# Kernel optimization log

Hardware: AMD Instinct MI355X
Metric: run time of the kernel (lower is better)

Reference implementation:

```python
import jax, jax.numpy as jnp
import numpy as np

B, S, D, H = 4, 2048, 512, 8
DEPTH = D // H


def setup_inputs() -> dict:
    key = jax.random.key(0)
    ks = jax.random.split(key, 12)
    s = 0.02
    return {
        "q": jax.random.normal(ks[0], (B, S, D), jnp.float32),
        "k": jax.random.normal(ks[1], (B, S, D), jnp.float32),
        "v": jax.random.normal(ks[2], (B, S, D), jnp.float32),
        "mask": jax.random.randint(ks[3], (B, 1, 1, S), 0, 2, jnp.int32),
        "wq": jax.random.normal(ks[4], (D, D), jnp.float32) * s,
        "bq": jnp.zeros((D,), jnp.float32),
        "wk": jax.random.normal(ks[5], (D, D), jnp.float32) * s,
        "bk": jnp.zeros((D,), jnp.float32),
        "wv": jax.random.normal(ks[6], (D, D), jnp.float32) * s,
        "bv": jnp.zeros((D,), jnp.float32),
        "wo": jax.random.normal(ks[7], (D, D), jnp.float32) * s,
        "bo": jnp.zeros((D,), jnp.float32),
    }


def _split_heads(x):
    # [B,S,D] -> [B,H,S,depth]
    b = x.shape[0]
    return x.reshape(b, -1, H, DEPTH).transpose(0, 2, 1, 3)


def reference(q, k, v, mask, wq, bq, wk, bk, wv, bv, wo, bo):
    qh = _split_heads(q @ wq + bq)
    kh = _split_heads(k @ wk + bk)
    vh = _split_heads(v @ wv + bv)
    scale = 1.0 / jnp.sqrt(jnp.float32(DEPTH))
    logits = jnp.einsum("bhqd,bhkd->bhqk", qh, kh) * scale
    logits = logits + mask.astype(jnp.float32) * -1e9
    attn = jax.nn.softmax(logits, axis=-1)  # [B,H,Sq,Sk]
    out = jnp.einsum("bhqk,bhkd->bhqd", attn, vh)
    out = out.transpose(0, 2, 1, 3).reshape(q.shape[0], -1, D)
    out = out @ wo + bo
    return out, attn
```

## Files before the change

kernel.cpp:

```cpp
#include <hip/hip_runtime.h>

#define B_ 4
#define S_ 2048
#define D_ 512
#define H_ 8
#define DP_ 64
#define NT_ (S_/64)

typedef __attribute__((ext_vector_type(4))) float f32x4;
typedef __attribute__((ext_vector_type(8))) short short8;
typedef __attribute__((ext_vector_type(4))) int i32x4;

__device__ __forceinline__ short f2bf(float f){
  unsigned u = __float_as_uint(f);
  u += 0x7fff + ((u >> 16) & 1);
  return (short)(u >> 16);
}

__device__ __forceinline__ int cvtpk(float lo, float hi){
  int r;
  asm("v_cvt_pk_bf16_f32 %0, %1, %2" : "=v"(r) : "v"(lo), "v"(hi));
  return r;
}

#define SWZ(r, kb) ((r)*64 + ((kb) ^ (((r)&7)<<3)))
#define F2(r) ((((r)&3)) | ((((r)>>3)&1)<<2))
#define SWZ2(r, kb) ((r)*64 + ((kb) ^ (F2(r)<<3)))

#define WAITV(N) do{ asm volatile("s_waitcnt vmcnt(" #N ")" ::: "memory"); }while(0)
#define BAR() do{ __builtin_amdgcn_s_barrier(); __builtin_amdgcn_sched_barrier(0); }while(0)

template<int NC>
__device__ __forceinline__ void stage_swz(const short* __restrict__ g, int rowStride,
                                          short* shbase, int w, int l){
  #pragma unroll
  for(int i = 0; i < NC; ++i){
    int byte = (w*NC + i)*1024 + l*16;
    int row = byte >> 7;
    int gs = ((byte >> 4) & 7) ^ (row & 7);
    const short* src = g + (size_t)row*rowStride + gs*8;
    __builtin_amdgcn_global_load_lds((const __attribute__((address_space(1))) void*)src,
        (__attribute__((address_space(3))) void*)(shbase + (w*NC + i)*512), 16, 0, 0);
  }
}
template<int NC>
__device__ __forceinline__ void stage_swz2(const short* __restrict__ g, int rowStride,
                                           short* shbase, int w, int l){
  #pragma unroll
  for(int i = 0; i < NC; ++i){
    int byte = (w*NC + i)*1024 + l*16;
    int row = byte >> 7;
    int gs = ((byte >> 4) & 7) ^ F2(row);
    const short* src = g + (size_t)row*rowStride + gs*8;
    __builtin_amdgcn_global_load_lds((const __attribute__((address_space(1))) void*)src,
        (__attribute__((address_space(3))) void*)(shbase + (w*NC + i)*512), 16, 0, 0);
  }
}

__global__ __launch_bounds__(256) void k_pre(const int* __restrict__ mask,
        const float* __restrict__ w0, const float* __restrict__ w1,
        const float* __restrict__ w2, const float* __restrict__ w3,
        short* __restrict__ wT, float* __restrict__ mb){
  __shared__ float tt[32][33];
  const int bi = blockIdx.x, t = threadIdx.x;
  if(bi < 1024){
    const int z = bi >> 8;
    const float* w = z == 0 ? w0 : z == 1 ? w1 : z == 2 ? w2 : w3;
    short* wt = wT + z * 262144;
    const int bxy = bi & 255;
    const int bx = (bxy & 15) * 32, by = (bxy >> 4) * 32;
    const int tx = t & 31, ty = t >> 5;
    #pragma unroll
    for(int i = 0; i < 32; i += 8) tt[ty + i][tx] = w[(by + ty + i) * D_ + bx + tx];
    __syncthreads();
    #pragma unroll
    for(int i = 0; i < 32; i += 8) wt[(bx + ty + i) * D_ + by + tx] = f2bf(tt[tx][ty + i]);
  } else {
    int i = (bi - 1024) * 256 + t;
    mb[i] = mask[i] ? -1.0e9f : 0.0f;
  }
}

__global__ __launch_bounds__(256) void k_gemm_qkv(const float* __restrict__ qf,
        const float* __restrict__ kf, const float* __restrict__ vf,
        const short* __restrict__ WTall, const float* __restrict__ b0,
        const float* __restrict__ b1, const float* __restrict__ b2,
        short* __restrict__ qh, short* __restrict__ kh, short* __restrict__ vvt){
  __shared__ __align__(16) short As[8192];
  __shared__ __align__(16) short Bs[8192];
  const int z = blockIdx.z;
  const float* X = z == 0 ? qf : (z == 1 ? kf : vf);
  const short* WT = WTall + (size_t)z * (D_*D_);
  const float* bias = z==0 ? b0 : (z==1 ? b1 : b2);
  const int t = threadIdx.x, l = t & 63, w = t >> 6;
  const int lr = l & 15, lg = l >> 4;
  const int m0 = blockIdx.x * 128, n0 = blockIdx.y * 128;
  const int wr = w >> 1, wc = w & 1;
  const float* Xb = X + (size_t)m0 * D_;
  const short* Wb = WT + (size_t)n0 * D_;
  f32x4 acc[4][4] = {};
  for(int kt = 0; kt < D_ / 64; ++kt){
    #pragma unroll
    for(int i = 0; i < 4; ++i){
      int e = t + 256 * i;
      int row = e >> 3, c8 = (e & 7) * 8;
      const float* src = Xb + (size_t)row * D_ + kt * 64 + c8;
      float4 f0 = *reinterpret_cast<const float4*>(src);
      float4 f1 = *reinterpret_cast<const float4*>(src + 4);
      i32x4 pk;
      pk[0] = cvtpk(f0.x, f0.y); pk[1] = cvtpk(f0.z, f0.w);
      pk[2] = cvtpk(f1.x, f1.y); pk[3] = cvtpk(f1.z, f1.w);
      *reinterpret_cast<i32x4*>(&As[SWZ(row, c8)]) = pk;
    }
    stage_swz<4>(Wb + kt*64, D_, Bs, w, l);
    __syncthreads();
    #pragma unroll
    for(int ks = 0; ks < 2; ++ks){
      const int kb = ks*32 + lg*8;
      short8 a[4], b[4];
      #pragma unroll
      for(int mt = 0; mt < 4; ++mt)
        a[mt] = *reinterpret_cast<const short8*>(&As[SWZ(wr*64 + mt*16 + lr, kb)]);
      #pragma unroll
      for(int nt = 0; nt < 4; ++nt)
        b[nt] = *reinterpret_cast<const short8*>(&Bs[SWZ(wc*64 + nt*16 + lr, kb)]);
      __builtin_amdgcn_s_setprio(1);
      #pragma unroll
      for(int mt = 0; mt < 4; ++mt)
        #pragma unroll
        for(int nt = 0; nt < 4; ++nt)
          acc[mt][nt] = __builtin_amdgcn_mfma_f32_16x16x32_bf16(a[mt], b[nt], acc[mt][nt], 0, 0, 0);
      __builtin_amdgcn_s_setprio(0);
    }
    __syncthreads();
  }
  #pragma unroll
  for(int mt = 0; mt < 4; ++mt){
    #pragma unroll
    for(int nt = 0; nt < 4; ++nt){
      const int n = n0 + wc*64 + nt*16 + lr;
      const int m4 = m0 + wr*64 + mt*16 + lg*4;
      float vals[4];
      #pragma unroll
      for(int r = 0; r < 4; ++r) vals[r] = acc[mt][nt][r] + bias[n];
      if(z == 2){
        short4 pv4;
        pv4.x = f2bf(vals[0]); pv4.y = f2bf(vals[1]); pv4.z = f2bf(vals[2]); pv4.w = f2bf(vals[3]);
        *reinterpret_cast<short4*>(&vvt[
            (((size_t)((m4 >> 11) * H_ + (n >> 6))) * DP_ + (n & 63)) * S_ + (m4 & 2047)]) = pv4;
      } else {
        short* dst = z == 0 ? qh : kh;
        #pragma unroll
        for(int r = 0; r < 4; ++r){
          int m = m4 + r;
          dst[(((size_t)((m >> 11) * H_ + (n >> 6))) * S_ + (m & 2047)) * DP_ + (n & 63)] = f2bf(vals[r]);
        }
      }
    }
  }
}

__global__ __launch_bounds__(256) void k_gemm_out(const short* __restrict__ X,
        const short* __restrict__ WT, const float* __restrict__ bias,
        float* __restrict__ Out){
  __shared__ __align__(16) short As[8192];
  __shared__ __align__(16) short Bs[8192];
  const int t = threadIdx.x, l = t & 63, w = t >> 6;
  const int lr = l & 15, lg = l >> 4;
  const int m0 = blockIdx.x * 128, n0 = blockIdx.y * 128;
  const int wr = w >> 1, wc = w & 1;
  const short* Xb = X + (size_t)m0 * D_;
  const short* Wb = WT + (size_t)n0 * D_;
  f32x4 acc[4][4] = {};
  for(int kt = 0; kt < D_ / 64; ++kt){
    stage_swz<4>(Xb + kt*64, D_, As, w, l);
    stage_swz<4>(Wb + kt*64, D_, Bs, w, l);
    __syncthreads();
    #pragma unroll
    for(int ks = 0; ks < 2; ++ks){
      const int kb = ks*32 + lg*8;
      short8 a[4], b[4];
      #pragma unroll
      for(int mt = 0; mt < 4; ++mt)
        a[mt] = *reinterpret_cast<const short8*>(&As[SWZ(wr*64 + mt*16 + lr, kb)]);
      #pragma unroll
      for(int nt = 0; nt < 4; ++nt)
        b[nt] = *reinterpret_cast<const short8*>(&Bs[SWZ(wc*64 + nt*16 + lr, kb)]);
      __builtin_amdgcn_s_setprio(1);
      #pragma unroll
      for(int mt = 0; mt < 4; ++mt)
        #pragma unroll
        for(int nt = 0; nt < 4; ++nt)
          acc[mt][nt] = __builtin_amdgcn_mfma_f32_16x16x32_bf16(a[mt], b[nt], acc[mt][nt], 0, 0, 0);
      __builtin_amdgcn_s_setprio(0);
    }
    __syncthreads();
  }
  #pragma unroll
  for(int mt = 0; mt < 4; ++mt){
    #pragma unroll
    for(int nt = 0; nt < 4; ++nt){
      const int n = n0 + wc*64 + nt*16 + lr;
      const int m4 = m0 + wr*64 + mt*16 + lg*4;
      #pragma unroll
      for(int r = 0; r < 4; ++r)
        Out[(size_t)(m4 + r) * D_ + n] = acc[mt][nt][r] + bias[n];
    }
  }
}

__global__ __launch_bounds__(512, 4) void k_attn(const short* __restrict__ qh,
                                                 const short* __restrict__ kh,
                                                 const short* __restrict__ vt,
                                                 const float* __restrict__ mb,
                                                 float* __restrict__ attn,
                                                 short* __restrict__ ctx){
  __shared__ __align__(16) short Sh[36864];
  const int t = threadIdx.x, l = t & 63, w = t >> 6;
  const int lr = l & 15, lg = l >> 4;
  int lin = blockIdx.y * 16 + blockIdx.x;
  int sw = (lin & 7) * 64 + (lin >> 3);
  const int bh = sw >> 4, b = bh >> 3, h = bh & 7;
  const int q0 = (sw & 15) * 128;
  const short* Qb = qh + (size_t)bh * S_ * DP_ + (size_t)q0 * DP_;
  const short* Kb = kh + (size_t)bh * S_ * DP_;
  const short* Vtb = vt + (size_t)bh * DP_ * S_;
  const float* Mbb = mb + b * S_;
  float* Mlds = (float*)Sh;
  short* KA = Sh + 4096;
  short* KB = Sh + 4096;
  short* VB = Sh + 20480;
  short* Qs = Sh + 28672;
  const float scale = 0.125f;

  __builtin_amdgcn_global_load_lds(
      (const __attribute__((address_space(1))) void*)(Mbb + w*256 + l*4),
      (__attribute__((address_space(3))) void*)(Mlds + w*256 + l*4), 16, 0, 0);
  stage_swz2<2>(Qb, DP_, Qs, w, l);
  stage_swz2<1>(Kb,            DP_, KA,            w, l);
  stage_swz2<1>(Kb + 4096,     DP_, KA + 4096,     w, l);
  stage_swz2<1>(Kb + 2*4096,   DP_, KA + 2*4096,   w, l);
  stage_swz2<1>(Kb + 3*4096,   DP_, KA + 3*4096,   w, l);
  WAITV(4); BAR();
  short8 bq0, bq1;
  {
    int r = w * 16 + lr;
    bq0 = *reinterpret_cast<const short8*>(&Qs[SWZ2(r, lg * 8)]);
    bq1 = *reinterpret_cast<const short8*>(&Qs[SWZ2(r, 32 + lg * 8)]);
  }
  const int grow = ((lr >> 2) << 3) + (lr & 3);

  float ps = 0.f;
  for(int i = 0; i < NT_/2; ++i){
    if(i < NT_/2 - 1){ WAITV(2); } else { WAITV(0); }
    BAR();
    if(i + 2 < NT_/2){
      int tfa = 2*i + 4, tfb = 2*i + 5;
      stage_swz2<1>(Kb + (size_t)tfa * 4096, DP_, KA + (tfa % 6) * 4096, w, l);
      stage_swz2<1>(Kb + (size_t)tfb * 4096, DP_, KA + (tfb % 6) * 4096, w, l);
    }
    #pragma unroll
    for(int tt = 0; tt < 2; ++tt){
      const int kt = 2*i + tt;
      const short* Kc = KA + (kt % 6) * 4096;
      const float* Ml = Mlds + kt * 64;
      #pragma unroll
      for(int st = 0; st < 4; ++st){
        const int ks = st >> 1, h4 = st & 1;
        const int row = grow + h4 * 4 + ks * 32;
        const int mcol = ks * 32 + h4 * 4 + lg * 8;
        const float4 mv = *(const float4*)&Ml[mcol];
        short8 ak0 = *reinterpret_cast<const short8*>(&Kc[SWZ2(row, lg * 8)]);
        short8 ak1 = *reinterpret_cast<const short8*>(&Kc[SWZ2(row, 32 + lg * 8)]);
        __builtin_amdgcn_s_setprio(1);
        f32x4 c = {};
        c = __builtin_amdgcn_mfma_f32_16x16x32_bf16(ak0, bq0, c, 0, 0, 0);
        c = __builtin_amdgcn_mfma_f32_16x16x32_bf16(ak1, bq1, c, 0, 0, 0);
        __builtin_amdgcn_s_setprio(0);
        ps += __expf(__builtin_fmaf(c[0], scale, mv.x));
        ps += __expf(__builtin_fmaf(c[1], scale, mv.y));
        ps += __expf(__builtin_fmaf(c[2], scale, mv.z));
        ps += __expf(__builtin_fmaf(c[3], scale, mv.w));
      }
    }
  }
  ps += __shfl_xor(ps, 16, 64);
  ps += __shfl_xor(ps, 32, 64);
  const float rinv = 1.f / ps;

  BAR();
  stage_swz2<1>(Kb,          DP_, KB,          w, l);
  stage_swz2<1>(Kb + 4096,   DP_, KB + 4096,   w, l);
  stage_swz2<1>(Vtb,         S_,  VB,          w, l);
  stage_swz2<1>(Vtb + 64,    S_,  VB + 4096,   w, l);
  stage_swz2<1>(Kb + 2*4096, DP_, KB + 2*4096, w, l);
  stage_swz2<1>(Kb + 3*4096, DP_, KB + 3*4096, w, l);
  stage_swz2<1>(Vtb + 2*64,  S_,  VB + 2*4096, w, l);
  stage_swz2<1>(Vtb + 3*64,  S_,  VB + 3*4096, w, l);

  f32x4 o[4] = {};
  for(int i = 0; i < NT_/2; ++i){
    if(i == 0){ WAITV(4); } else { WAITV(8); }
    BAR();
    if(i >= 1 && i + 1 < NT_/2){
      int tfa = 2*i + 2, tfb = 2*i + 3;
      stage_swz2<1>(Kb + (size_t)tfa * 4096, DP_, KB + (tfa & 3) * 4096, w, l);
      stage_swz2<1>(Kb + (size_t)tfb * 4096, DP_, KB + (tfb & 3) * 4096, w, l);
      stage_swz2<1>(Vtb + (size_t)tfa * 64,  S_,  VB + (tfa & 3) * 4096, w, l);
      stage_swz2<1>(Vtb + (size_t)tfb * 64,  S_,  VB + (tfb & 3) * 4096, w, l);
    }
    #pragma unroll
    for(int tt = 0; tt < 2; ++tt){
      const int kt = 2*i + tt;
      const short* Kc = KB + (kt & 3) * 4096;
      const short* Vc = VB + (kt & 3) * 4096;
      const float* Ml = Mlds + kt * 64;
      const int q = q0 + w * 16 + lr;
      i32x4 pav[2];
      #pragma unroll
      for(int st = 0; st < 4; ++st){
        const int ks = st >> 1, h4 = st & 1;
        const int row = grow + h4 * 4 + ks * 32;
        const int mcol = ks * 32 + h4 * 4 + lg * 8;
        const float4 mv = *(const float4*)&Ml[mcol];
        short8 ak0 = *reinterpret_cast<const short8*>(&Kc[SWZ2(row, lg * 8)]);
        short8 ak1 = *reinterpret_cast<const short8*>(&Kc[SWZ2(row, 32 + lg * 8)]);
        __builtin_amdgcn_s_setprio(1);
        f32x4 c = {};
        c = __builtin_amdgcn_mfma_f32_16x16x32_bf16(ak0, bq0, c, 0, 0, 0);
        c = __builtin_amdgcn_mfma_f32_16x16x32_bf16(ak1, bq1, c, 0, 0, 0);
        __builtin_amdgcn_s_setprio(0);
        float4 pw;
        pw.x = __expf(__builtin_fmaf(c[0], scale, mv.x)) * rinv;
        pw.y = __expf(__builtin_fmaf(c[1], scale, mv.y)) * rinv;
        pw.z = __expf(__builtin_fmaf(c[2], scale, mv.z)) * rinv;
        pw.w = __expf(__builtin_fmaf(c[3], scale, mv.w)) * rinv;
        *reinterpret_cast<float4*>(&attn[((size_t)bh * S_ + q) * S_ + kt * 64 + mcol]) = pw;
        pav[ks][h4 * 2 + 0] = cvtpk(pw.x, pw.y);
        pav[ks][h4 * 2 + 1] = cvtpk(pw.z, pw.w);
      }
      #pragma unroll
      for(int ks = 0; ks < 2; ++ks){
        short8 pa = __builtin_bit_cast(short8, pav[ks]);
        __builtin_amdgcn_s_setprio(1);
        #pragma unroll
        for(int dt = 0; dt < 4; ++dt){
          short8 vb = *reinterpret_cast<const short8*>(&Vc[SWZ2(dt * 16 + lr, ks * 32 + lg * 8)]);
          o[dt] = __builtin_amdgcn_mfma_f32_16x16x32_bf16(pa, vb, o[dt], 0, 0, 0);
        }
        __builtin_amdgcn_s_setprio(0);
      }
    }
  }
  #pragma unroll
  for(int dt = 0; dt < 4; ++dt){
    #pragma unroll
    for(int r = 0; r < 4; ++r){
      int q = q0 + w * 16 + lg * 4 + r;
      int dd = h * 64 + dt * 16 + lr;
      ctx[((size_t)b * S_ + q) * D_ + dd] = f2bf(o[dt][r]);
    }
  }
}

extern "C" void kernel_launch(void* const* d_in, const int* in_sizes, int n_in,
                              void* d_out, int out_size, void* d_ws, size_t ws_size,
                              hipStream_t stream){
  const float* q  = (const float*)d_in[0];
  const float* k  = (const float*)d_in[1];
  const float* v  = (const float*)d_in[2];
  const int* mask = (const int*)d_in[3];
  const float* wq = (const float*)d_in[4];
  const float* bq = (const float*)d_in[5];
  const float* wk = (const float*)d_in[6];
  const float* bk = (const float*)d_in[7];
  const float* wv = (const float*)d_in[8];
  const float* bv = (const float*)d_in[9];
  const float* wo = (const float*)d_in[10];
  const float* bo = (const float*)d_in[11];

  float* out  = (float*)d_out;
  float* attn = out + (size_t)B_ * S_ * D_;

  char* ws = (char*)d_ws;
  short* qh  = (short*)(ws);
  short* kh  = (short*)(ws + 8388608);
  short* vvt = (short*)(ws + 16777216);
  short* ctx = (short*)(ws + 25165824);
  short* wT  = (short*)(ws + 33554432);
  float* mb  = (float*)(ws + 33554432 + 4 * 524288);

  hipLaunchKernelGGL(k_pre, dim3(1056), dim3(256), 0, stream,
                     mask, wq, wk, wv, wo, wT, mb);

  hipLaunchKernelGGL(k_gemm_qkv, dim3(64, 4, 3), dim3(256), 0, stream,
                     q, k, v, wT, bq, bk, bv, qh, kh, vvt);

  hipLaunchKernelGGL(k_attn, dim3(16, 32), dim3(512), 0, stream, qh, kh, vvt, mb, attn, ctx);

  hipLaunchKernelGGL(k_gemm_out, dim3(64, 4), dim3(256), 0, stream, ctx, wT + 3 * 262144, bo, out);
}
```

Before: 223.9 us.

## Process two query sub-tiles per wave in attention to reuse K/V tiles

Each attention block now covers 256 queries instead of 128, with every wave computing two 16-row query sub-tiles that share the same K and V fragments read from LDS. This halves the number of blocks and the K/V global-to-LDS staging per query, cutting memory traffic for keys and values. In exchange, register use roughly doubles for accumulators, the launch bound drops to 2 blocks per CU, and only 256 blocks remain, which may hurt occupancy and latency hiding. The kernel is dominated by writing the large attn probability matrix, so the gain from reuse may be limited.

```diff
diff --git a/kernel.cpp b/kernel.cpp
--- a/kernel.cpp
+++ b/kernel.cpp
@@ -209,19 +209,19 @@
   }
 }
 
-__global__ __launch_bounds__(512, 4) void k_attn(const short* __restrict__ qh,
+__global__ __launch_bounds__(512, 2) void k_attn(const short* __restrict__ qh,
                                                  const short* __restrict__ kh,
                                                  const short* __restrict__ vt,
                                                  const float* __restrict__ mb,
                                                  float* __restrict__ attn,
                                                  short* __restrict__ ctx){
-  __shared__ __align__(16) short Sh[36864];
+  __shared__ __align__(16) short Sh[45056];
   const int t = threadIdx.x, l = t & 63, w = t >> 6;
   const int lr = l & 15, lg = l >> 4;
-  int lin = blockIdx.y * 16 + blockIdx.x;
-  int sw = (lin & 7) * 64 + (lin >> 3);
-  const int bh = sw >> 4, b = bh >> 3, h = bh & 7;
-  const int q0 = (sw & 15) * 128;
+  int lin = blockIdx.y * 8 + blockIdx.x;
+  int sw = (lin & 7) * 32 + (lin >> 3);
+  const int bh = sw >> 3, b = bh >> 3, h = bh & 7;
+  const int q0 = (sw & 7) * 256;
   const short* Qb = qh + (size_t)bh * S_ * DP_ + (size_t)q0 * DP_;
   const short* Kb = kh + (size_t)bh * S_ * DP_;
   const short* Vtb = vt + (size_t)bh * DP_ * S_;
@@ -236,21 +236,22 @@
   __builtin_amdgcn_global_load_lds(
       (const __attribute__((address_space(1))) void*)(Mbb + w*256 + l*4),
       (__attribute__((address_space(3))) void*)(Mlds + w*256 + l*4), 16, 0, 0);
-  stage_swz2<2>(Qb, DP_, Qs, w, l);
-  stage_swz2<1>(Kb,            DP_, KA,            w, l);
-  stage_swz2<1>(Kb + 4096,     DP_, KA + 4096,     w, l);
-  stage_swz2<1>(Kb + 2*4096,   DP_, KA + 2*4096,   w, l);
-  stage_swz2<1>(Kb + 3*4096,   DP_, KA + 3*4096,   w, l);
+  stage_swz2<4>(Qb, DP_, Qs, w, l);
+  stage_swz2<1>(Kb,          DP_, KA,          w, l);
+  stage_swz2<1>(Kb + 4096,   DP_, KA + 4096,   w, l);
+  stage_swz2<1>(Kb + 2*4096, DP_, KA + 2*4096, w, l);
+  stage_swz2<1>(Kb + 3*4096, DP_, KA + 3*4096, w, l);
   WAITV(4); BAR();
-  short8 bq0, bq1;
-  {
-    int r = w * 16 + lr;
-    bq0 = *reinterpret_cast<const short8*>(&Qs[SWZ2(r, lg * 8)]);
-    bq1 = *reinterpret_cast<const short8*>(&Qs[SWZ2(r, 32 + lg * 8)]);
+  short8 bq[2][2];
+  #pragma unroll
+  for(int qs = 0; qs < 2; ++qs){
+    int r = w * 32 + qs * 16 + lr;
+    bq[qs][0] = *reinterpret_cast<const short8*>(&Qs[SWZ2(r, lg * 8)]);
+    bq[qs][1] = *reinterpret_cast<const short8*>(&Qs[SWZ2(r, 32 + lg * 8)]);
   }
   const int grow = ((lr >> 2) << 3) + (lr & 3);
 
-  float ps = 0.f;
+  float ps[2] = {0.f, 0.f};
   for(int i = 0; i < NT_/2; ++i){
     if(i < NT_/2 - 1){ WAITV(2); } else { WAITV(0); }
     BAR();
@@ -273,20 +274,29 @@
         short8 ak0 = *reinterpret_cast<const short8*>(&Kc[SWZ2(row, lg * 8)]);
         short8 ak1 = *reinterpret_cast<const short8*>(&Kc[SWZ2(row, 32 + lg * 8)]);
         __builtin_amdgcn_s_setprio(1);
-        f32x4 c = {};
-        c = __builtin_amdgcn_mfma_f32_16x16x32_bf16(ak0, bq0, c, 0, 0, 0);
-        c = __builtin_amdgcn_mfma_f32_16x16x32_bf16(ak1, bq1, c, 0, 0, 0);
+        f32x4 c0 = {}, c1 = {};
+        c0 = __builtin_amdgcn_mfma_f32_16x16x32_bf16(ak0, bq[0][0], c0, 0, 0, 0);
+        c0 = __builtin_amdgcn_mfma_f32_16x16x32_bf16(ak1, bq[0][1], c0, 0, 0, 0);
+        c1 = __builtin_amdgcn_mfma_f32_16x16x32_bf16(ak0, bq[1][0], c1, 0, 0, 0);
+        c1 = __builtin_amdgcn_mfma_f32_16x16x32_bf16(ak1, bq[1][1], c1, 0, 0, 0);
         __builtin_amdgcn_s_setprio(0);
-        ps += __expf(__builtin_fmaf(c[0], scale, mv.x));
-        ps += __expf(__builtin_fmaf(c[1], scale, mv.y));
-        ps += __expf(__builtin_fmaf(c[2], scale, mv.z));
-        ps += __expf(__builtin_fmaf(c[3], scale, mv.w));
+        ps[0] += __expf(__builtin_fmaf(c0[0], scale, mv.x));
+        ps[0] += __expf(__builtin_fmaf(c0[1], scale, mv.y));
+        ps[0] += __expf(__builtin_fmaf(c0[2], scale, mv.z));
+        ps[0] += __expf(__builtin_fmaf(c0[3], scale, mv.w));
+        ps[1] += __expf(__builtin_fmaf(c1[0], scale, mv.x));
+        ps[1] += __expf(__builtin_fmaf(c1[1], scale, mv.y));
+        ps[1] += __expf(__builtin_fmaf(c1[2], scale, mv.z));
+        ps[1] += __expf(__builtin_fmaf(c1[3], scale, mv.w));
       }
     }
   }
-  ps += __shfl_xor(ps, 16, 64);
-  ps += __shfl_xor(ps, 32, 64);
-  const float rinv = 1.f / ps;
+  #pragma unroll
+  for(int qs = 0; qs < 2; ++qs){
+    ps[qs] += __shfl_xor(ps[qs], 16, 64);
+    ps[qs] += __shfl_xor(ps[qs], 32, 64);
+  }
+  const float rinv0 = 1.f / ps[0], rinv1 = 1.f / ps[1];
 
   BAR();
   stage_swz2<1>(Kb,          DP_, KB,          w, l);
@@ -298,9 +308,9 @@
   stage_swz2<1>(Vtb + 2*64,  S_,  VB + 2*4096, w, l);
   stage_swz2<1>(Vtb + 3*64,  S_,  VB + 3*4096, w, l);
 
-  f32x4 o[4] = {};
+  f32x4 o[2][4] = {};
   for(int i = 0; i < NT_/2; ++i){
-    if(i == 0){ WAITV(4); } else { WAITV(8); }
+    if(i == 0){ WAITV(4); } else { WAITV(16); }
     BAR();
     if(i >= 1 && i + 1 < NT_/2){
       int tfa = 2*i + 2, tfb = 2*i + 3;
@@ -315,8 +325,7 @@
       const short* Kc = KB + (kt & 3) * 4096;
       const short* Vc = VB + (kt & 3) * 4096;
       const float* Ml = Mlds + kt * 64;
-      const int q = q0 + w * 16 + lr;
-      i32x4 pav[2];
+      i32x4 pav[2][2];
       #pragma unroll
       for(int st = 0; st < 4; ++st){
         const int ks = st >> 1, h4 = st & 1;
@@ -326,39 +335,54 @@
         short8 ak0 = *reinterpret_cast<const short8*>(&Kc[SWZ2(row, lg * 8)]);
         short8 ak1 = *reinterpret_cast<const short8*>(&Kc[SWZ2(row, 32 + lg * 8)]);
         __builtin_amdgcn_s_setprio(1);
-        f32x4 c = {};
-        c = __builtin_amdgcn_mfma_f32_16x16x32_bf16(ak0, bq0, c, 0, 0, 0);
-        c = __builtin_amdgcn_mfma_f32_16x16x32_bf16(ak1, bq1, c, 0, 0, 0);
+        f32x4 c0 = {}, c1 = {};
+        c0 = __builtin_amdgcn_mfma_f32_16x16x32_bf16(ak0, bq[0][0], c0, 0, 0, 0);
+        c0 = __builtin_amdgcn_mfma_f32_16x16x32_bf16(ak1, bq[0][1], c0, 0, 0, 0);
+        c1 = __builtin_amdgcn_mfma_f32_16x16x32_bf16(ak0, bq[1][0], c1, 0, 0, 0);
+        c1 = __builtin_amdgcn_mfma_f32_16x16x32_bf16(ak1, bq[1][1], c1, 0, 0, 0);
         __builtin_amdgcn_s_setprio(0);
-        float4 pw;
-        pw.x = __expf(__builtin_fmaf(c[0], scale, mv.x)) * rinv;
-        pw.y = __expf(__builtin_fmaf(c[1], scale, mv.y)) * rinv;
-        pw.z = __expf(__builtin_fmaf(c[2], scale, mv.z)) * rinv;
-        pw.w = __expf(__builtin_fmaf(c[3], scale, mv.w)) * rinv;
-        *reinterpret_cast<float4*>(&attn[((size_t)bh * S_ + q) * S_ + kt * 64 + mcol]) = pw;
-        pav[ks][h4 * 2 + 0] = cvtpk(pw.x, pw.y);
-        pav[ks][h4 * 2 + 1] = cvtpk(pw.z, pw.w);
+        float4 pw0, pw1;
+        pw0.x = __expf(__builtin_fmaf(c0[0], scale, mv.x)) * rinv0;
+        pw0.y = __expf(__builtin_fmaf(c0[1], scale, mv.y)) * rinv0;
+        pw0.z = __expf(__builtin_fmaf(c0[2], scale, mv.z)) * rinv0;
+        pw0.w = __expf(__builtin_fmaf(c0[3], scale, mv.w)) * rinv0;
+        pw1.x = __expf(__builtin_fmaf(c1[0], scale, mv.x)) * rinv1;
+        pw1.y = __expf(__builtin_fmaf(c1[1], scale, mv.y)) * rinv1;
+        pw1.z = __expf(__builtin_fmaf(c1[2], scale, mv.z)) * rinv1;
+        pw1.w = __expf(__builtin_fmaf(c1[3], scale, mv.w)) * rinv1;
+        const int q0r = q0 + w * 32 + lr;
+        *reinterpret_cast<float4*>(&attn[((size_t)bh * S_ + q0r) * S_ + kt * 64 + mcol]) = pw0;
+        *reinterpret_cast<float4*>(&attn[((size_t)bh * S_ + q0r + 16) * S_ + kt * 64 + mcol]) = pw1;
+        pav[0][ks][h4 * 2 + 0] = cvtpk(pw0.x, pw0.y);
+        pav[0][ks][h4 * 2 + 1] = cvtpk(pw0.z, pw0.w);
+        pav[1][ks][h4 * 2 + 0] = cvtpk(pw1.x, pw1.y);
+        pav[1][ks][h4 * 2 + 1] = cvtpk(pw1.z, pw1.w);
       }
       #pragma unroll
       for(int ks = 0; ks < 2; ++ks){
-        short8 pa = __builtin_bit_cast(short8, pav[ks]);
+        short8 pa0 = __builtin_bit_cast(short8, pav[0][ks]);
+        short8 pa1 = __builtin_bit_cast(short8, pav[1][ks]);
         __builtin_amdgcn_s_setprio(1);
         #pragma unroll
         for(int dt = 0; dt < 4; ++dt){
           short8 vb = *reinterpret_cast<const short8*>(&Vc[SWZ2(dt * 16 + lr, ks * 32 + lg * 8)]);
-          o[dt] = __builtin_amdgcn_mfma_f32_16x16x32_bf16(pa, vb, o[dt], 0, 0, 0);
+          o[0][dt] = __builtin_amdgcn_mfma_f32_16x16x32_bf16(pa0, vb, o[0][dt], 0, 0, 0);
+          o[1][dt] = __builtin_amdgcn_mfma_f32_16x16x32_bf16(pa1, vb, o[1][dt], 0, 0, 0);
         }
         __builtin_amdgcn_s_setprio(0);
       }
     }
   }
   #pragma unroll
-  for(int dt = 0; dt < 4; ++dt){
-    #pragma unroll
-    for(int r = 0; r < 4; ++r){
-      int q = q0 + w * 16 + lg * 4 + r;
-      int dd = h * 64 + dt * 16 + lr;
-      ctx[((size_t)b * S_ + q) * D_ + dd] = f2bf(o[dt][r]);
+  for(int qs = 0; qs < 2; ++qs){
+    #pragma unroll
+    for(int dt = 0; dt < 4; ++dt){
+      #pragma unroll
+      for(int r = 0; r < 4; ++r){
+        int q = q0 + w * 32 + qs * 16 + lg * 4 + r;
+        int dd = h * 64 + dt * 16 + lr;
+        ctx[((size_t)b * S_ + q) * D_ + dd] = f2bf(o[qs][dt][r]);
+      }
     }
   }
 }
@@ -396,7 +420,7 @@
   hipLaunchKernelGGL(k_gemm_qkv, dim3(64, 4, 3), dim3(256), 0, stream,
                      q, k, v, wT, bq, bk, bv, qh, kh, vvt);
 
-  hipLaunchKernelGGL(k_attn, dim3(16, 32), dim3(512), 0, stream, qh, kh, vvt, mb, attn, ctx);
+  hipLaunchKernelGGL(k_attn, dim3(8, 32), dim3(512), 0, stream, qh, kh, vvt, mb, attn, ctx);
 
   hipLaunchKernelGGL(k_gemm_out, dim3(64, 4), dim3(256), 0, stream, ctx, wT + 3 * 262144, bo, out);
 }
```

After: 251.5 us. +12.3%, slower.
